# Kernel tuning notes

Measured on AMD Instinct MI355X. Metric: run time of the kernel, lower is better.

Reference implementation:

```python
import jax, jax.numpy as jnp
import numpy as np
from jax import lax

WINDOW_SIZE = 12
POOL = 4  # AvgPool2d(4): 12x12 -> 3x3

# 4 directional 3x3 kernels, stacked as [O=4, I=1, 3, 3]
_KERNELS = np.stack([
    np.array([[0, 0, 0], [-1, 1, 0], [0, 0, 0]], np.float32),  # left
    np.array([[0, 0, 0], [0, 1, -1], [0, 0, 0]], np.float32),  # right
    np.array([[0, -1, 0], [0, 1, 0], [0, 0, 0]], np.float32),  # up
    np.array([[0, 0, 0], [0, 1, 0], [0, -1, 0]], np.float32),  # down
])[:, None, :, :]


def setup_inputs() -> dict:
    key = jax.random.key(0)
    k1, k2 = jax.random.split(key)
    windows_num = 200000
    n = WINDOW_SIZE * WINDOW_SIZE * windows_num
    samples1 = jax.random.uniform(k1, (n, 3), dtype=jnp.float32)
    samples2 = jax.random.uniform(k2, (n, 3), dtype=jnp.float32)
    return {"samples1": samples1, "samples2": samples2, "windows_num": windows_num}


def _to_pooled(samples, windows_num):
    # [W*W*N, C] -> [W, W, N, C] -> [N, C, W, W]
    x = samples.reshape(WINDOW_SIZE, WINDOW_SIZE, windows_num, -1)
    x = jnp.transpose(x, (2, 3, 0, 1))
    # channel mean, keepdim -> [N, 1, W, W]
    m = jnp.mean(x, axis=1, keepdims=True)
    # AvgPool2d(4): [N,1,12,12] -> [N,1,3,3]
    hp = WINDOW_SIZE // POOL
    p = m.reshape(windows_num, 1, hp, POOL, hp, POOL).mean(axis=(3, 5))
    return p


def _dir_grads(x):
    # x: [N,1,3,3]; 4 directional 3x3 convs, padding=1 -> [N,4,3,3]
    k = jnp.asarray(_KERNELS)
    return lax.conv_general_dilated(
        x, k, window_strides=(1, 1), padding=[(1, 1), (1, 1)],
        dimension_numbers=("NCHW", "OIHW", "NCHW"))


def reference(samples1, samples2, windows_num):
    org_pool = _to_pooled(samples1, windows_num)
    enh_pool = _to_pooled(samples2, windows_num)
    d_org = _dir_grads(org_pool)
    d_enh = _dir_grads(enh_pool)
    # squared diff per direction, summed over the 4 directions -> [N,3,3]
    E = jnp.sum((d_org - d_enh) ** 2, axis=1)
    return jnp.mean(E)
```

## Files before the change

kernel.cpp:

```cpp
#include <hip/hip_runtime.h>

__global__ __launch_bounds__(256) void spa_kernel(
    const float* __restrict__ s1, const float* __restrict__ s2,
    float* __restrict__ out, int N, float scale) {
  const int lane = threadIdx.x & 63;
  const int rg   = threadIdx.x >> 6;
  const int win  = blockIdx.x * 64 + lane;

  float rowacc[3][3];
#pragma unroll
  for (int a = 0; a < 3; ++a)
#pragma unroll
    for (int b = 0; b < 3; ++b) rowacc[a][b] = 0.f;

  if (win < N) {
    const size_t stride = (size_t)N * 3u;
    const float* p1 = s1 + (size_t)win * 3u;
    const float* p2 = s2 + (size_t)win * 3u;
#pragma unroll
    for (int ii = 0; ii < 3; ++ii) {
      const int i = rg * 3 + ii;
      const float* q1 = p1 + (size_t)(i * 12) * stride;
      const float* q2 = p2 + (size_t)(i * 12) * stride;
#pragma unroll
      for (int j = 0; j < 12; ++j) {
        const float* a = q1 + (size_t)j * stride;
        const float* b = q2 + (size_t)j * stride;
        float d = (a[0] + a[1] + a[2]) - (b[0] + b[1] + b[2]);
        rowacc[ii][j >> 2] += d;
      }
    }
  }

  __shared__ float sRow[12][64][3];
#pragma unroll
  for (int ii = 0; ii < 3; ++ii) {
    const int i = rg * 3 + ii;
#pragma unroll
    for (int c = 0; c < 3; ++c) sRow[i][lane][c] = rowacc[ii][c];
  }
  __syncthreads();

  if (rg == 0) {
    float P[9];
#pragma unroll
    for (int p = 0; p < 3; ++p)
#pragma unroll
      for (int c = 0; c < 3; ++c) {
        float v = sRow[4 * p][lane][c] + sRow[4 * p + 1][lane][c] +
                  sRow[4 * p + 2][lane][c] + sRow[4 * p + 3][lane][c];
        P[p * 3 + c] = v * (1.0f / 48.0f);
      }

    float e = 0.f;
#pragma unroll
    for (int i = 0; i < 3; ++i) {
#pragma unroll
      for (int j = 0; j < 3; ++j) {
        float c = P[i * 3 + j];
        float l = (j > 0) ? P[i * 3 + j - 1] : 0.f;
        float r = (j < 2) ? P[i * 3 + j + 1] : 0.f;
        float u = (i > 0) ? P[(i - 1) * 3 + j] : 0.f;
        float d = (i < 2) ? P[(i + 1) * 3 + j] : 0.f;
        float dl = c - l, dr = c - r, du = c - u, dd = c - d;
        e += dl * dl + dr * dr + du * du + dd * dd;
      }
    }

#pragma unroll
    for (int off = 32; off > 0; off >>= 1) e += __shfl_down(e, off, 64);
    if (lane == 0) atomicAdd(out, e * scale);
  }
}

extern "C" void kernel_launch(void* const* d_in, const int* in_sizes, int n_in,
                              void* d_out, int out_size, void* d_ws, size_t ws_size,
                              hipStream_t stream) {
  const float* s1 = (const float*)d_in[0];
  const float* s2 = (const float*)d_in[1];
  float* out = (float*)d_out;
  int N = in_sizes[0] / (12 * 12 * 3);
  float scale = 1.0f / (9.0f * (float)N);
  hipMemsetAsync(d_out, 0, sizeof(float), stream);
  int blocks = (N + 63) / 64;
  spa_kernel<<<blocks, 256, 0, stream>>>(s1, s2, out, N, scale);
}
```

Measured before the change: 644.6 us.

## Assign one full window per thread and reduce atomics per block

Each thread now handles all 12 rows of its window instead of splitting rows across four warps, which removes the shared-memory staging and the idle warps in the energy phase. Blocks grow to 512 windows, with a two-level shuffle and shared reduction, so there is one atomic per 512 windows instead of one per 64. The trade-off is fewer threads in flight and a serial row loop (unroll 1), which lowers memory-level parallelism in a kernel that is bandwidth-bound.

```diff
diff --git a/kernel.cpp b/kernel.cpp
--- a/kernel.cpp
+++ b/kernel.cpp
@@ -1,75 +1,64 @@
 #include <hip/hip_runtime.h>
 
-__global__ __launch_bounds__(256) void spa_kernel(
+__global__ __launch_bounds__(512) void spa_kernel(
     const float* __restrict__ s1, const float* __restrict__ s2,
     float* __restrict__ out, int N, float scale) {
-  const int lane = threadIdx.x & 63;
-  const int rg   = threadIdx.x >> 6;
-  const int win  = blockIdx.x * 64 + lane;
+  const int win = blockIdx.x * 512 + threadIdx.x;
 
-  float rowacc[3][3];
+  float P[9];
 #pragma unroll
-  for (int a = 0; a < 3; ++a)
-#pragma unroll
-    for (int b = 0; b < 3; ++b) rowacc[a][b] = 0.f;
+  for (int k = 0; k < 9; ++k) P[k] = 0.f;
 
   if (win < N) {
     const size_t stride = (size_t)N * 3u;
     const float* p1 = s1 + (size_t)win * 3u;
     const float* p2 = s2 + (size_t)win * 3u;
-#pragma unroll
-    for (int ii = 0; ii < 3; ++ii) {
-      const int i = rg * 3 + ii;
-      const float* q1 = p1 + (size_t)(i * 12) * stride;
-      const float* q2 = p2 + (size_t)(i * 12) * stride;
+#pragma unroll 1
+    for (int i = 0; i < 12; ++i) {
+      const int pr = (i >> 2) * 3;
 #pragma unroll
       for (int j = 0; j < 12; ++j) {
-        const float* a = q1 + (size_t)j * stride;
-        const float* b = q2 + (size_t)j * stride;
+        const float* a = p1 + (size_t)j * stride;
+        const float* b = p2 + (size_t)j * stride;
         float d = (a[0] + a[1] + a[2]) - (b[0] + b[1] + b[2]);
-        rowacc[ii][j >> 2] += d;
+        P[pr + (j >> 2)] += d;
       }
+      p1 += (size_t)12 * stride;
+      p2 += (size_t)12 * stride;
     }
   }
 
-  __shared__ float sRow[12][64][3];
 #pragma unroll
-  for (int ii = 0; ii < 3; ++ii) {
-    const int i = rg * 3 + ii;
+  for (int k = 0; k < 9; ++k) P[k] *= (1.0f / 48.0f);
+
+  float e = 0.f;
 #pragma unroll
-    for (int c = 0; c < 3; ++c) sRow[i][lane][c] = rowacc[ii][c];
+  for (int i = 0; i < 3; ++i) {
+#pragma unroll
+    for (int j = 0; j < 3; ++j) {
+      float c = P[i * 3 + j];
+      float l = (j > 0) ? P[i * 3 + j - 1] : 0.f;
+      float r = (j < 2) ? P[i * 3 + j + 1] : 0.f;
+      float u = (i > 0) ? P[(i - 1) * 3 + j] : 0.f;
+      float d = (i < 2) ? P[(i + 1) * 3 + j] : 0.f;
+      float dl = c - l, dr = c - r, du = c - u, dd = c - d;
+      e += dl * dl + dr * dr + du * du + dd * dd;
+    }
   }
+
+  const int lane = threadIdx.x & 63;
+  const int wid = threadIdx.x >> 6;
+#pragma unroll
+  for (int off = 32; off > 0; off >>= 1) e += __shfl_down(e, off, 64);
+
+  __shared__ float sPart[8];
+  if (lane == 0) sPart[wid] = e;
   __syncthreads();
-
-  if (rg == 0) {
-    float P[9];
+  if (threadIdx.x == 0) {
+    float t = 0.f;
 #pragma unroll
-    for (int p = 0; p < 3; ++p)
-#pragma unroll
-      for (int c = 0; c < 3; ++c) {
-        float v = sRow[4 * p][lane][c] + sRow[4 * p + 1][lane][c] +
-                  sRow[4 * p + 2][lane][c] + sRow[4 * p + 3][lane][c];
-        P[p * 3 + c] = v * (1.0f / 48.0f);
-      }
-
-    float e = 0.f;
-#pragma unroll
-    for (int i = 0; i < 3; ++i) {
-#pragma unroll
-      for (int j = 0; j < 3; ++j) {
-        float c = P[i * 3 + j];
-        float l = (j > 0) ? P[i * 3 + j - 1] : 0.f;
-        float r = (j < 2) ? P[i * 3 + j + 1] : 0.f;
-        float u = (i > 0) ? P[(i - 1) * 3 + j] : 0.f;
-        float d = (i < 2) ? P[(i + 1) * 3 + j] : 0.f;
-        float dl = c - l, dr = c - r, du = c - u, dd = c - d;
-        e += dl * dl + dr * dr + du * du + dd * dd;
-      }
-    }
-
-#pragma unroll
-    for (int off = 32; off > 0; off >>= 1) e += __shfl_down(e, off, 64);
-    if (lane == 0) atomicAdd(out, e * scale);
+    for (int w = 0; w < 8; ++w) t += sPart[w];
+    atomicAdd(out, t * scale);
   }
 }
 
@@ -82,6 +71,6 @@
   int N = in_sizes[0] / (12 * 12 * 3);
   float scale = 1.0f / (9.0f * (float)N);
   hipMemsetAsync(d_out, 0, sizeof(float), stream);
-  int blocks = (N + 63) / 64;
-  spa_kernel<<<blocks, 256, 0, stream>>>(s1, s2, out, N, scale);
+  int blocks = (N + 511) / 512;
+  spa_kernel<<<blocks, 512, 0, stream>>>(s1, s2, out, N, scale);
 }
```

Measured after the change: 643.2 us. About the same (-0.2%).
